# Optimization experiments

Measured on AMD Instinct MI355X. Metric: run time of the kernel, lower is better.

Reference implementation:

```python
import jax, jax.numpy as jnp
import numpy as np

B, D = 8192, 8          # batch, number of input features (= number of TT cores)
P = 10                  # poly_deg + 1 (basis width per feature)
R = 512                 # fixed TT rank
OUT = 64                # output dim (dims[0])
N_MID = D - 2           # middle cores
U_LO, U_HI = -0.1, 0.1  # uniform init range


def setup_inputs() -> dict:
    key = jax.random.key(0)
    kz, k0, km, kl = jax.random.split(key, 4)
    z = jax.random.normal(kz, (B, D), dtype=jnp.float32)
    G0 = jax.random.uniform(k0, (P, R), minval=U_LO, maxval=U_HI, dtype=jnp.float32)
    G_mid = jax.random.uniform(km, (N_MID, R, P, R), minval=U_LO, maxval=U_HI, dtype=jnp.float32)
    G_last = jax.random.uniform(kl, (R, P, OUT), minval=U_LO, maxval=U_HI, dtype=jnp.float32)
    return {"z": z, "G0": G0, "G_mid": G_mid, "G_last": G_last, "t": 0}


def _poly_basis(z, p):
    # Phi[i] = [z_i^0, ..., z_i^(p-1)]  -> stacked as [B, D, P]
    return z[:, :, None] ** jnp.arange(p, dtype=z.dtype)


def reference(z, G0, G_mid, G_last, t):
    phi = _poly_basis(z, G0.shape[0])                 # [B, D, P]
    # first core: tanh(G0)[j, r], Phi0[b, j] -> res[b, r]
    res = jnp.einsum('jr,bj->br', jnp.tanh(G0), phi[:, 0, :])
    # middle cores: res[b,i] . tanh(G)[i,j,k] . Phi[b,j] -> [b,k]
    for i in range(G_mid.shape[0]):
        tmp = jnp.einsum('bi,ijk->bjk', res, jnp.tanh(G_mid[i]))   # [B, P, R]
        res = jnp.einsum('bjk,bj->bk', tmp, phi[:, i + 1, :])      # [B, R]
    # last core -> output dim
    tmp = jnp.einsum('bi,ijl->bjl', res, jnp.tanh(G_last))         # [B, P, OUT]
    res = jnp.einsum('bjl,bj->bl', tmp, phi[:, -1, :])             # [B, OUT]
    return res
```

## Files before the change

### kernel.cpp

```cpp
#include <hip/hip_runtime.h>
#include <hip/hip_bf16.h>
#include <stdint.h>

#define BB   8192
#define DD   8
#define PP   10
#define RR   512
#define OUTD 64
#define KK   5120

typedef __bf16 bf16x8 __attribute__((ext_vector_type(8)));
typedef float  f32x4  __attribute__((ext_vector_type(4)));

template <int N>
__global__ __launch_bounds__(256) void frag_pack(
        const float* __restrict__ G, __hip_bfloat16* __restrict__ dst, int ldi) {
    constexpr int LOGN = (N == 512) ? 9 : 6;
    __shared__ __hip_bfloat16 sT[32 * (N + 8)];
    const int kc = blockIdx.x, j = blockIdx.y, c = blockIdx.z;
    const float* Gp = G + (size_t)c * 512 * ldi;
    __hip_bfloat16* db = dst + (size_t)c * 5120 * N + (size_t)(j * 16 + kc) * 32 * N;
    #pragma unroll
    for (int e = 0; e < N / 32; ++e) {
        const int idx = (e * 256 + threadIdx.x) * 4;
        const int row = idx >> LOGN, col = idx & (N - 1);
        f32x4 v = *(const f32x4*)(Gp + (size_t)(kc * 32 + row) * ldi + (size_t)j * N + col);
        __hip_bfloat16* sp = sT + row * (N + 8) + col;
        sp[0] = __float2bfloat16(tanhf(v.x));
        sp[1] = __float2bfloat16(tanhf(v.y));
        sp[2] = __float2bfloat16(tanhf(v.z));
        sp[3] = __float2bfloat16(tanhf(v.w));
    }
    __syncthreads();
    #pragma unroll
    for (int cc = 0; cc < N / 64; ++cc) {
        const int ch = cc * 256 + threadIdx.x;
        const int nt = ch >> 6, l = ch & 63;
        const int r0 = (l >> 4) * 8, cb = nt * 16 + (l & 15);
        union { __hip_bfloat16 h[8]; uint4 u; } pk;
        #pragma unroll
        for (int e = 0; e < 8; ++e) pk.h[e] = sT[(r0 + e) * (N + 8) + cb];
        *(uint4*)(db + (size_t)ch * 8) = pk.u;
    }
}

__global__ __launch_bounds__(512) void tanh_g0(
        const float* __restrict__ G0, float* __restrict__ tG0) {
    const int i = blockIdx.x * 512 + threadIdx.x;
    tG0[i] = tanhf(G0[i]);
}

__global__ __launch_bounds__(512) void tt_first(
        const float* __restrict__ z, const float* __restrict__ tG0,
        __hip_bfloat16* __restrict__ res0) {
    const int r = threadIdx.x;
    const int b0 = blockIdx.x * 32;
    float tg[10];
    #pragma unroll
    for (int j = 0; j < 10; ++j) tg[j] = tG0[j * RR + r];
    #pragma unroll 1
    for (int b = 0; b < 32; ++b) {
        const float z0 = z[(size_t)(b0 + b) * DD];
        float acc = tg[9];
        #pragma unroll
        for (int j = 8; j >= 0; --j) acc = acc * z0 + tg[j];
        res0[(size_t)(b0 + b) * RR + r] = __float2bfloat16(acc);
    }
}

template <bool LASTV, int NTOT, int MT>
__global__ __launch_bounds__(256, 2) void tt_gemm_ks(
        const __hip_bfloat16* __restrict__ resin,
        const __hip_bfloat16* __restrict__ tBf,
        void* __restrict__ outp,
        const float* __restrict__ z, int d) {
    __shared__ f32x4 red[2][MT * 4][64];

    const int tid  = threadIdx.x;
    const int lane = tid & 63;
    const int wave = tid >> 6;
    const int m0 = LASTV ? blockIdx.x * (MT * 16) : (blockIdx.x >> 3) * 64;
    const int nb = LASTV ? 0 : (blockIdx.x & 7);
    const int r16 = lane & 15, quad = lane >> 4;

    bf16x8 a[MT * 4];
    #pragma unroll
    for (int ms = 0; ms < MT; ++ms)
        #pragma unroll
        for (int kst = 0; kst < 4; ++kst)
            a[ms * 4 + kst] = *(const bf16x8*)(
                resin + (size_t)(m0 + ms * 16 + r16) * RR + wave * 128 + kst * 32 + quad * 8);

    float zr[MT * 4];
    #pragma unroll
    for (int ms = 0; ms < MT; ++ms)
        #pragma unroll
        for (int r = 0; r < 4; ++r)
            zr[ms * 4 + r] = z[(size_t)(m0 + ms * 16 + quad * 4 + r) * DD + d];

    f32x4 acc[MT][4];
    #pragma unroll
    for (int ms = 0; ms < MT; ++ms)
        #pragma unroll
        for (int sn = 0; sn < 4; ++sn) acc[ms][sn] = f32x4{0.f, 0.f, 0.f, 0.f};

    constexpr size_t SK = (size_t)NTOT * 512;
    constexpr size_t PJ = 16 * SK;
    const __hip_bfloat16* pB = tBf + (size_t)nb * 4 * 512
                             + (size_t)wave * 4 * SK + (size_t)lane * 8;

    bf16x8 bv[4][4];
    #pragma unroll
    for (int s = 0; s < 3; ++s)
        #pragma unroll
        for (int sn = 0; sn < 4; ++sn)
            bv[s][sn] = *(const bf16x8*)(pB + (size_t)9 * PJ + (size_t)s * SK + sn * 512);

#define MFMA_STEP(SLOT)                                                        \
    _Pragma("unroll")                                                          \
    for (int ms = 0; ms < MT; ++ms)                                            \
        _Pragma("unroll")                                                      \
        for (int sn = 0; sn < 4; ++sn)                                         \
            acc[ms][sn] = __builtin_amdgcn_mfma_f32_16x16x32_bf16(             \
                a[ms * 4 + SLOT], bv[SLOT][sn], acc[ms][sn], 0, 0, 0);

    #pragma unroll 1
    for (int p = 0; p < 10; ++p) {
        const int j = 9 - p;
        if (p) {
            #pragma unroll
            for (int ms = 0; ms < MT; ++ms)
                #pragma unroll
                for (int sn = 0; sn < 4; ++sn)
                    #pragma unroll
                    for (int r = 0; r < 4; ++r)
                        acc[ms][sn][r] *= zr[ms * 4 + r];
        }
        const size_t jb = (size_t)j * PJ;
        #pragma unroll
        for (int sn = 0; sn < 4; ++sn)
            bv[3][sn] = *(const bf16x8*)(pB + jb + (size_t)3 * SK + sn * 512);
        MFMA_STEP(0)
        if (p < 9) {
            #pragma unroll
            for (int sn = 0; sn < 4; ++sn)
                bv[0][sn] = *(const bf16x8*)(pB + jb - PJ + sn * 512);
        }
        MFMA_STEP(1)
        if (p < 9) {
            #pragma unroll
            for (int sn = 0; sn < 4; ++sn)
                bv[1][sn] = *(const bf16x8*)(pB + jb - PJ + SK + sn * 512);
        }
        MFMA_STEP(2)
        if (p < 9) {
            #pragma unroll
            for (int sn = 0; sn < 4; ++sn)
                bv[2][sn] = *(const bf16x8*)(pB + jb - PJ + 2 * SK + sn * 512);
        }
        MFMA_STEP(3)
    }
#undef MFMA_STEP

    if (wave & 1) {
        const int idx = wave >> 1;
        #pragma unroll
        for (int i = 0; i < MT * 4; ++i) red[idx][i][lane] = acc[i >> 2][i & 3];
    }
    __syncthreads();
    if (wave == 0) {
        #pragma unroll
        for (int i = 0; i < MT * 4; ++i) acc[i >> 2][i & 3] += red[0][i][lane];
    }
    if (wave == 2) {
        #pragma unroll
        for (int i = 0; i < MT * 4; ++i) {
            f32x4 t = acc[i >> 2][i & 3] + red[1][i][lane];
            red[1][i][lane] = t;
        }
    }
    __syncthreads();
    float* rc = (float*)&red[0][0][0];
    if (wave == 0) {
        #pragma unroll
        for (int i = 0; i < MT * 4; ++i) acc[i >> 2][i & 3] += red[1][i][lane];
        #pragma unroll
        for (int ms = 0; ms < MT; ++ms)
            #pragma unroll
            for (int sn = 0; sn < 4; ++sn)
                #pragma unroll
                for (int r = 0; r < 4; ++r)
                    rc[(ms * 16 + quad * 4 + r) * 64 + sn * 16 + r16] = acc[ms][sn][r];
    }
    __syncthreads();

    if (LASTV) {
        float* o = (float*)outp;
        const int row = tid >> 3, cg = (tid & 7) * 8;
        #pragma unroll
        for (int q = 0; q < 2; ++q)
            *(f32x4*)(o + (size_t)(m0 + row) * OUTD + cg + q * 4) =
                *(const f32x4*)(rc + row * 64 + cg + q * 4);
    } else {
        __hip_bfloat16* o = (__hip_bfloat16*)outp;
        const int row = tid >> 2, cg = (tid & 3) * 16;
        #pragma unroll
        for (int h = 0; h < 2; ++h) {
            union { __hip_bfloat16 hh[8]; uint4 u; } pk;
            #pragma unroll
            for (int e = 0; e < 8; ++e)
                pk.hh[e] = __float2bfloat16(rc[row * 64 + cg + h * 8 + e]);
            *(uint4*)(o + (size_t)(m0 + row) * RR + nb * 64 + cg + h * 8) = pk.u;
        }
    }
}

extern "C" void kernel_launch(void* const* d_in, const int* in_sizes, int n_in,
                              void* d_out, int out_size, void* d_ws, size_t ws_size,
                              hipStream_t stream) {
    const float* z     = (const float*)d_in[0];
    const float* G0    = (const float*)d_in[1];
    const float* Gmid  = (const float*)d_in[2];
    const float* Glast = (const float*)d_in[3];
    float* out = (float*)d_out;

    char* ws = (char*)d_ws;
    __hip_bfloat16* resX   = (__hip_bfloat16*)ws;
    __hip_bfloat16* resY   = (__hip_bfloat16*)(ws + ((size_t)8 << 20));
    __hip_bfloat16* tBf    = (__hip_bfloat16*)(ws + ((size_t)16 << 20));
    __hip_bfloat16* tBlf   = (__hip_bfloat16*)(ws + ((size_t)48 << 20));
    float* tG0             = (float*)(ws + ((size_t)52 << 20));

    frag_pack<512><<<dim3(16, 10, 6), 256, 0, stream>>>(Gmid,  tBf,  PP * RR);
    frag_pack<64> <<<dim3(16, 10, 1), 256, 0, stream>>>(Glast, tBlf, PP * OUTD);
    tanh_g0<<<dim3(10), 512, 0, stream>>>(G0, tG0);
    tt_first<<<dim3(BB / 32), 512, 0, stream>>>(z, tG0, resX);

    __hip_bfloat16* rin = resX;
    __hip_bfloat16* rnext = resY;
    for (int c = 0; c < 6; ++c) {
        tt_gemm_ks<false, 32, 4><<<dim3(1024), 256, 0, stream>>>(
            rin, tBf + (size_t)c * RR * KK, rnext, z, c + 1);
        __hip_bfloat16* t = rin; rin = rnext; rnext = t;
    }
    tt_gemm_ks<true, 4, 2><<<dim3(BB / 32), 256, 0, stream>>>(
        rin, tBlf, out, z, 7);
}
```

Before: 399.6 us.

## Fuse weight prep kernels, remap GEMM grid, use nontemporal B loads on odd cores

Merges the three preprocessing launches (mid-core packing, last-core packing, tanh of G0) into a single kernel to cut launch overhead. Changes the middle GEMM grid from a 1D index split into (M-tile, N-tile) to a 2D grid with blockIdx.x over M. Under the usual dispatch order this makes consecutive blocks share an N-slice of B rather than an M-tile of activations, which alters L2 reuse. On alternating cores the B-fragment loads use nontemporal hints, presumably to keep activations resident in cache. The 2D grid and the nontemporal path trade one kind of cache reuse for another, so the net effect could go either way.

Result: slower. 434.7 us (+8.8%).

```diff
diff --git a/kernel.cpp b/kernel.cpp
--- a/kernel.cpp
+++ b/kernel.cpp
@@ -12,42 +12,79 @@
 typedef __bf16 bf16x8 __attribute__((ext_vector_type(8)));
 typedef float  f32x4  __attribute__((ext_vector_type(4)));
 
-template <int N>
-__global__ __launch_bounds__(256) void frag_pack(
-        const float* __restrict__ G, __hip_bfloat16* __restrict__ dst, int ldi) {
-    constexpr int LOGN = (N == 512) ? 9 : 6;
-    __shared__ __hip_bfloat16 sT[32 * (N + 8)];
-    const int kc = blockIdx.x, j = blockIdx.y, c = blockIdx.z;
-    const float* Gp = G + (size_t)c * 512 * ldi;
-    __hip_bfloat16* db = dst + (size_t)c * 5120 * N + (size_t)(j * 16 + kc) * 32 * N;
-    #pragma unroll
-    for (int e = 0; e < N / 32; ++e) {
-        const int idx = (e * 256 + threadIdx.x) * 4;
-        const int row = idx >> LOGN, col = idx & (N - 1);
-        f32x4 v = *(const f32x4*)(Gp + (size_t)(kc * 32 + row) * ldi + (size_t)j * N + col);
-        __hip_bfloat16* sp = sT + row * (N + 8) + col;
-        sp[0] = __float2bfloat16(tanhf(v.x));
-        sp[1] = __float2bfloat16(tanhf(v.y));
-        sp[2] = __float2bfloat16(tanhf(v.z));
-        sp[3] = __float2bfloat16(tanhf(v.w));
-    }
-    __syncthreads();
-    #pragma unroll
-    for (int cc = 0; cc < N / 64; ++cc) {
-        const int ch = cc * 256 + threadIdx.x;
-        const int nt = ch >> 6, l = ch & 63;
-        const int r0 = (l >> 4) * 8, cb = nt * 16 + (l & 15);
-        union { __hip_bfloat16 h[8]; uint4 u; } pk;
-        #pragma unroll
-        for (int e = 0; e < 8; ++e) pk.h[e] = sT[(r0 + e) * (N + 8) + cb];
-        *(uint4*)(db + (size_t)ch * 8) = pk.u;
-    }
-}
-
-__global__ __launch_bounds__(512) void tanh_g0(
-        const float* __restrict__ G0, float* __restrict__ tG0) {
-    const int i = blockIdx.x * 512 + threadIdx.x;
-    tG0[i] = tanhf(G0[i]);
+template <bool NT>
+__device__ __forceinline__ bf16x8 ldb(const __hip_bfloat16* p) {
+    if constexpr (NT) return __builtin_nontemporal_load((const bf16x8*)p);
+    else              return *(const bf16x8*)p;
+}
+
+__global__ __launch_bounds__(256) void prep_fused(
+        const float* __restrict__ Gmid, const float* __restrict__ Glast,
+        const float* __restrict__ G0,
+        __hip_bfloat16* __restrict__ tBf, __hip_bfloat16* __restrict__ tBlf,
+        float* __restrict__ tG0) {
+    __shared__ __hip_bfloat16 sT[32 * 520];
+    const int u = blockIdx.x, tid = threadIdx.x;
+    if (u < 960) {
+        const int c = u / 160, rem = u - c * 160;
+        const int j = rem >> 4, kc = rem & 15;
+        const float* Gp = Gmid + (size_t)c * (512 * 5120);
+        __hip_bfloat16* db = tBf + (size_t)c * (RR * KK)
+                           + (size_t)(j * 16 + kc) * 16384;
+        #pragma unroll
+        for (int e = 0; e < 16; ++e) {
+            const int idx = (e * 256 + tid) * 4;
+            const int row = idx >> 9, col = idx & 511;
+            f32x4 v = *(const f32x4*)(Gp + (size_t)(kc * 32 + row) * 5120
+                                      + (size_t)j * 512 + col);
+            __hip_bfloat16* sp = sT + row * 520 + col;
+            sp[0] = __float2bfloat16(tanhf(v.x));
+            sp[1] = __float2bfloat16(tanhf(v.y));
+            sp[2] = __float2bfloat16(tanhf(v.z));
+            sp[3] = __float2bfloat16(tanhf(v.w));
+        }
+        __syncthreads();
+        #pragma unroll
+        for (int cc = 0; cc < 8; ++cc) {
+            const int ch = cc * 256 + tid;
+            const int nt = ch >> 6, l = ch & 63;
+            const int r0 = (l >> 4) * 8, cb = nt * 16 + (l & 15);
+            union { __hip_bfloat16 h[8]; uint4 u4; } pk;
+            #pragma unroll
+            for (int e = 0; e < 8; ++e) pk.h[e] = sT[(r0 + e) * 520 + cb];
+            *(uint4*)(db + (size_t)ch * 8) = pk.u4;
+        }
+    } else if (u < 970) {
+        const int j = u - 960;
+        #pragma unroll 1
+        for (int kc = 0; kc < 16; ++kc) {
+            __syncthreads();
+            #pragma unroll
+            for (int it = 0; it < 2; ++it) {
+                const int idx = (it * 256 + tid) * 4;
+                const int row = idx >> 6, col = idx & 63;
+                f32x4 v = *(const f32x4*)(Glast + (size_t)(kc * 32 + row) * 640
+                                          + (size_t)j * 64 + col);
+                __hip_bfloat16* sp = sT + row * 72 + col;
+                sp[0] = __float2bfloat16(tanhf(v.x));
+                sp[1] = __float2bfloat16(tanhf(v.y));
+                sp[2] = __float2bfloat16(tanhf(v.z));
+                sp[3] = __float2bfloat16(tanhf(v.w));
+            }
+            __syncthreads();
+            {
+                const int ch = tid;
+                const int nt = ch >> 6, l = ch & 63;
+                const int r0 = (l >> 4) * 8, cb = nt * 16 + (l & 15);
+                union { __hip_bfloat16 h[8]; uint4 u4; } pk;
+                #pragma unroll
+                for (int e = 0; e < 8; ++e) pk.h[e] = sT[(r0 + e) * 72 + cb];
+                *(uint4*)(tBlf + (size_t)(j * 16 + kc) * 2048 + (size_t)ch * 8) = pk.u4;
+            }
+        }
+    } else {
+        for (int x = tid; x < 5120; x += 256) tG0[x] = tanhf(G0[x]);
+    }
 }
 
 __global__ __launch_bounds__(512) void tt_first(
@@ -68,7 +105,7 @@
     }
 }
 
-template <bool LASTV, int NTOT, int MT>
+template <bool LASTV, int NTOT, int MT, bool NTB>
 __global__ __launch_bounds__(256, 2) void tt_gemm_ks(
         const __hip_bfloat16* __restrict__ resin,
         const __hip_bfloat16* __restrict__ tBf,
@@ -79,8 +116,8 @@
     const int tid  = threadIdx.x;
     const int lane = tid & 63;
     const int wave = tid >> 6;
-    const int m0 = LASTV ? blockIdx.x * (MT * 16) : (blockIdx.x >> 3) * 64;
-    const int nb = LASTV ? 0 : (blockIdx.x & 7);
+    const int m0 = LASTV ? blockIdx.x * (MT * 16) : blockIdx.x * 64;
+    const int nb = LASTV ? 0 : blockIdx.y;
     const int r16 = lane & 15, quad = lane >> 4;
 
     bf16x8 a[MT * 4];
@@ -114,7 +151,7 @@
     for (int s = 0; s < 3; ++s)
         #pragma unroll
         for (int sn = 0; sn < 4; ++sn)
-            bv[s][sn] = *(const bf16x8*)(pB + (size_t)9 * PJ + (size_t)s * SK + sn * 512);
+            bv[s][sn] = ldb<NTB>(pB + (size_t)9 * PJ + (size_t)s * SK + sn * 512);
 
 #define MFMA_STEP(SLOT)                                                        \
     _Pragma("unroll")                                                          \
@@ -139,24 +176,24 @@
         const size_t jb = (size_t)j * PJ;
         #pragma unroll
         for (int sn = 0; sn < 4; ++sn)
-            bv[3][sn] = *(const bf16x8*)(pB + jb + (size_t)3 * SK + sn * 512);
+            bv[3][sn] = ldb<NTB>(pB + jb + (size_t)3 * SK + sn * 512);
         MFMA_STEP(0)
         if (p < 9) {
             #pragma unroll
             for (int sn = 0; sn < 4; ++sn)
-                bv[0][sn] = *(const bf16x8*)(pB + jb - PJ + sn * 512);
+                bv[0][sn] = ldb<NTB>(pB + jb - PJ + sn * 512);
         }
         MFMA_STEP(1)
         if (p < 9) {
             #pragma unroll
             for (int sn = 0; sn < 4; ++sn)
-                bv[1][sn] = *(const bf16x8*)(pB + jb - PJ + SK + sn * 512);
+                bv[1][sn] = ldb<NTB>(pB + jb - PJ + SK + sn * 512);
         }
         MFMA_STEP(2)
         if (p < 9) {
             #pragma unroll
             for (int sn = 0; sn < 4; ++sn)
-                bv[2][sn] = *(const bf16x8*)(pB + jb - PJ + 2 * SK + sn * 512);
+                bv[2][sn] = ldb<NTB>(pB + jb - PJ + 2 * SK + sn * 512);
         }
         MFMA_STEP(3)
     }
@@ -225,24 +262,26 @@
     float* out = (float*)d_out;
 
     char* ws = (char*)d_ws;
-    __hip_bfloat16* resX   = (__hip_bfloat16*)ws;
-    __hip_bfloat16* resY   = (__hip_bfloat16*)(ws + ((size_t)8 << 20));
-    __hip_bfloat16* tBf    = (__hip_bfloat16*)(ws + ((size_t)16 << 20));
-    __hip_bfloat16* tBlf   = (__hip_bfloat16*)(ws + ((size_t)48 << 20));
-    float* tG0             = (float*)(ws + ((size_t)52 << 20));
-
-    frag_pack<512><<<dim3(16, 10, 6), 256, 0, stream>>>(Gmid,  tBf,  PP * RR);
-    frag_pack<64> <<<dim3(16, 10, 1), 256, 0, stream>>>(Glast, tBlf, PP * OUTD);
-    tanh_g0<<<dim3(10), 512, 0, stream>>>(G0, tG0);
+    __hip_bfloat16* resX = (__hip_bfloat16*)ws;
+    __hip_bfloat16* resY = (__hip_bfloat16*)(ws + ((size_t)8 << 20));
+    __hip_bfloat16* tBf  = (__hip_bfloat16*)(ws + ((size_t)16 << 20));
+    __hip_bfloat16* tBlf = (__hip_bfloat16*)(ws + ((size_t)48 << 20));
+    float* tG0           = (float*)(ws + ((size_t)49 << 20));
+
+    prep_fused<<<dim3(971), 256, 0, stream>>>(Gmid, Glast, G0, tBf, tBlf, tG0);
     tt_first<<<dim3(BB / 32), 512, 0, stream>>>(z, tG0, resX);
 
     __hip_bfloat16* rin = resX;
     __hip_bfloat16* rnext = resY;
     for (int c = 0; c < 6; ++c) {
-        tt_gemm_ks<false, 32, 4><<<dim3(1024), 256, 0, stream>>>(
-            rin, tBf + (size_t)c * RR * KK, rnext, z, c + 1);
+        if (c & 1)
+            tt_gemm_ks<false, 32, 4, true><<<dim3(BB / 64, RR / 64), 256, 0, stream>>>(
+                rin, tBf + (size_t)c * RR * KK, rnext, z, c + 1);
+        else
+            tt_gemm_ks<false, 32, 4, false><<<dim3(BB / 64, RR / 64), 256, 0, stream>>>(
+                rin, tBf + (size_t)c * RR * KK, rnext, z, c + 1);
         __hip_bfloat16* t = rin; rin = rnext; rnext = t;
     }
-    tt_gemm_ks<true, 4, 2><<<dim3(BB / 32), 256, 0, stream>>>(
+    tt_gemm_ks<true, 4, 2, false><<<dim3(BB / 32), 256, 0, stream>>>(
         rin, tBlf, out, z, 7);
 }
```
